# Kernel tuning notes

Hardware: AMD Instinct MI355X
Metric: run time of the kernel (lower is better)

## Reference

```python
import jax, jax.numpy as jnp
import numpy as np

POOL = 7  # pool_size
NUM_ROIS = 512


def setup_inputs() -> dict:
    key = jax.random.key(0)
    k1, k2, k3 = jax.random.split(key, 3)
    img = jax.random.normal(k1, (1, 64, 64, 1024), dtype=jnp.float32)
    xy = jax.random.randint(k2, (NUM_ROIS, 2), 0, 32)   # x1, y1
    wh = jax.random.randint(k3, (NUM_ROIS, 2), 4, 33)   # w, h >= 4 so crops are non-empty
    rois = jnp.concatenate([xy, wh], axis=1).astype(jnp.int32)  # [R,4] (x,y,w,h)
    return {"img": img, "rois": rois}


def _axis_coords(start, eff, pool):
    """Bilinear sample coords for tf.image.resize (half-pixel centers).
    start, eff: [R] int crop origin / effective extent along one axis.
    Returns lo/hi gather indices [R,pool] into the FULL image, and frac [R,pool].
    """
    eff_f = eff.astype(jnp.float32)[:, None]                     # [R,1]
    t = (jnp.arange(pool, dtype=jnp.float32) + 0.5)[None, :] * eff_f / pool - 0.5  # [R,pool]
    f0 = jnp.floor(t)
    frac = t - f0                                                # lerp weight (from unclamped floor, as in TF)
    i0 = jnp.clip(f0, 0.0, eff_f - 1.0).astype(jnp.int32) + start[:, None]
    i1 = jnp.clip(f0 + 1.0, 0.0, eff_f - 1.0).astype(jnp.int32) + start[:, None]
    return i0, i1, frac


def reference(img, rois):
    # img: [B,H,W,C] float32, rois: [R,4] int32 (x,y,w,h). Output: [B,R,P,P,C].
    B, H, W, C = img.shape
    x1, y1, w, h = rois[:, 0], rois[:, 1], rois[:, 2], rois[:, 3]
    we = jnp.minimum(x1 + w, W) - x1   # x2 = min(x1+w, W) as in source
    he = jnp.minimum(y1 + h, H) - y1
    yi0, yi1, fy = _axis_coords(y1, he, POOL)   # [R,P]
    xi0, xi1, fx = _axis_coords(x1, we, POOL)
    # One-shot gather of the 4 bilinear corners for all ROIs/pixels: [B,R,P,P,C]
    v00 = img[:, yi0[:, :, None], xi0[:, None, :], :]
    v01 = img[:, yi0[:, :, None], xi1[:, None, :], :]
    v10 = img[:, yi1[:, :, None], xi0[:, None, :], :]
    v11 = img[:, yi1[:, :, None], xi1[:, None, :], :]
    fx_b = fx[None, :, None, :, None]  # broadcast over [B,R,P(y),P(x),C]
    fy_b = fy[None, :, :, None, None]
    top = v00 + (v01 - v00) * fx_b
    bot = v10 + (v11 - v10) * fx_b
    return top + (bot - top) * fy_b
```

## Files before the change

### kernel.cpp

```cpp
#include <hip/hip_runtime.h>


#define POOLSZ 7
#define NROIS  512
#define IMG_H  64
#define IMG_W  64
#define IMG_C  1024
#define NSLAB  8
#define SLABC  (IMG_C / NSLAB)
#define CELLS  (POOLSZ * POOLSZ)

typedef float fvec4 __attribute__((ext_vector_type(4)));

__global__ __launch_bounds__(256) void roi_pool_slab_kernel(
    const float* __restrict__ img,
    const int*   __restrict__ rois,
    float*       __restrict__ out)
{
    const int bid  = blockIdx.x;
    const int slab = bid & (NSLAB - 1);
    const int r    = bid >> 3;

    const int x1 = rois[r * 4 + 0];
    const int y1 = rois[r * 4 + 1];
    const int w  = rois[r * 4 + 2];
    const int h  = rois[r * 4 + 3];

    const int we = min(x1 + w, IMG_W) - x1;
    const int he = min(y1 + h, IMG_H) - y1;
    const float wef = (float)we;
    const float hef = (float)he;

    const int g    = threadIdx.x >> 5;
    const int lane = threadIdx.x & 31;
    const int c    = slab * SLABC + lane * 4;

    #pragma unroll
    for (int iter = 0; iter < 7; ++iter) {
        const int cell = iter * 8 + g;
        if (cell < CELLS) {
            const int py = cell / POOLSZ;
            const int px = cell % POOLSZ;

            const float ty  = (py + 0.5f) * hef / (float)POOLSZ - 0.5f;
            const float fy0 = floorf(ty);
            const float fy  = ty - fy0;
            const int yi0 = (int)fminf(fmaxf(fy0,        0.0f), hef - 1.0f) + y1;
            const int yi1 = (int)fminf(fmaxf(fy0 + 1.0f, 0.0f), hef - 1.0f) + y1;

            const float tx  = (px + 0.5f) * wef / (float)POOLSZ - 0.5f;
            const float fx0 = floorf(tx);
            const float fx  = tx - fx0;
            const int xi0 = (int)fminf(fmaxf(fx0,        0.0f), wef - 1.0f) + x1;
            const int xi1 = (int)fminf(fmaxf(fx0 + 1.0f, 0.0f), wef - 1.0f) + x1;

            const size_t base00 = ((size_t)(yi0 * IMG_W + xi0)) * IMG_C + c;
            const size_t base01 = ((size_t)(yi0 * IMG_W + xi1)) * IMG_C + c;
            const size_t base10 = ((size_t)(yi1 * IMG_W + xi0)) * IMG_C + c;
            const size_t base11 = ((size_t)(yi1 * IMG_W + xi1)) * IMG_C + c;

            const fvec4 v00 = *reinterpret_cast<const fvec4*>(img + base00);
            const fvec4 v01 = *reinterpret_cast<const fvec4*>(img + base01);
            const fvec4 v10 = *reinterpret_cast<const fvec4*>(img + base10);
            const fvec4 v11 = *reinterpret_cast<const fvec4*>(img + base11);

            const fvec4 top = v00 + (v01 - v00) * fx;
            const fvec4 bot = v10 + (v11 - v10) * fx;
            const fvec4 o   = top + (bot - top) * fy;

            const size_t obase = ((size_t)(r * CELLS + cell)) * IMG_C + c;
            __builtin_nontemporal_store(o, reinterpret_cast<fvec4*>(out + obase));
        }
    }
}

extern "C" void kernel_launch(void* const* d_in, const int* in_sizes, int n_in,
                              void* d_out, int out_size, void* d_ws, size_t ws_size,
                              hipStream_t stream) {
    const float* img  = (const float*)d_in[0];
    const int*   rois = (const int*)d_in[1];
    float*       out  = (float*)d_out;

    const int nblocks = NROIS * NSLAB;
    roi_pool_slab_kernel<<<nblocks, 256, 0, stream>>>(img, rois, out);
}
```

Baseline: 27.63 us.

## Process four ROIs per block with shared-memory precomputed bilinear coordinates

Each block now handles four ROIs for one channel slab, with all 256 threads packed densely over ROI×cell×lane units. The old mapping left the last iteration with only one of eight warp groups active. Per-axis sample indices and lerp fractions are computed once into shared memory instead of per cell per thread. This adds a __syncthreads, shared-memory lookups and integer divides per unit, and cuts the block count by four, which may reduce latency hiding.

Result: faster. 27.05 us (-2.1%).

```diff
diff --git a/kernel.cpp b/kernel.cpp
--- a/kernel.cpp
+++ b/kernel.cpp
@@ -9,50 +9,76 @@
 #define NSLAB  8
 #define SLABC  (IMG_C / NSLAB)
 #define CELLS  (POOLSZ * POOLSZ)
+#define RPB    4
+#define UNITS  (RPB * CELLS * 32)
+#define ITERS  ((UNITS + 255) / 256)
 
 typedef float fvec4 __attribute__((ext_vector_type(4)));
 
-__global__ __launch_bounds__(256) void roi_pool_slab_kernel(
+__global__ __launch_bounds__(256) void roi_pool_kernel(
     const float* __restrict__ img,
     const int*   __restrict__ rois,
     float*       __restrict__ out)
 {
-    const int bid  = blockIdx.x;
-    const int slab = bid & (NSLAB - 1);
-    const int r    = bid >> 3;
+    __shared__ int   sYi0[RPB][POOLSZ], sYi1[RPB][POOLSZ];
+    __shared__ float sFy [RPB][POOLSZ];
+    __shared__ int   sXi0[RPB][POOLSZ], sXi1[RPB][POOLSZ];
+    __shared__ float sFx [RPB][POOLSZ];
 
-    const int x1 = rois[r * 4 + 0];
-    const int y1 = rois[r * 4 + 1];
-    const int w  = rois[r * 4 + 2];
-    const int h  = rois[r * 4 + 3];
+    const int bid     = blockIdx.x;
+    const int slab    = bid & (NSLAB - 1);
+    const int roibase = (bid >> 3) * RPB;
 
-    const int we = min(x1 + w, IMG_W) - x1;
-    const int he = min(y1 + h, IMG_H) - y1;
-    const float wef = (float)we;
-    const float hef = (float)he;
+    const int t = threadIdx.x;
 
-    const int g    = threadIdx.x >> 5;
-    const int lane = threadIdx.x & 31;
-    const int c    = slab * SLABC + lane * 4;
+    if (t < RPB * 2 * POOLSZ) {
+        const int rl   = t / (2 * POOLSZ);
+        const int j    = t % (2 * POOLSZ);
+        const int axis = j / POOLSZ;
+        const int p    = j % POOLSZ;
+        const int r    = roibase + rl;
 
-    #pragma unroll
-    for (int iter = 0; iter < 7; ++iter) {
-        const int cell = iter * 8 + g;
-        if (cell < CELLS) {
-            const int py = cell / POOLSZ;
-            const int px = cell % POOLSZ;
+        const int x1 = rois[r * 4 + 0];
+        const int y1 = rois[r * 4 + 1];
+        const int w  = rois[r * 4 + 2];
+        const int h  = rois[r * 4 + 3];
 
-            const float ty  = (py + 0.5f) * hef / (float)POOLSZ - 0.5f;
-            const float fy0 = floorf(ty);
-            const float fy  = ty - fy0;
-            const int yi0 = (int)fminf(fmaxf(fy0,        0.0f), hef - 1.0f) + y1;
-            const int yi1 = (int)fminf(fmaxf(fy0 + 1.0f, 0.0f), hef - 1.0f) + y1;
+        const int start = axis ? x1 : y1;
+        const int lim   = axis ? IMG_W : IMG_H;
+        const int ext   = axis ? w : h;
+        const int eff   = min(start + ext, lim) - start;
+        const float efff = (float)eff;
 
-            const float tx  = (px + 0.5f) * wef / (float)POOLSZ - 0.5f;
-            const float fx0 = floorf(tx);
-            const float fx  = tx - fx0;
-            const int xi0 = (int)fminf(fmaxf(fx0,        0.0f), wef - 1.0f) + x1;
-            const int xi1 = (int)fminf(fmaxf(fx0 + 1.0f, 0.0f), wef - 1.0f) + x1;
+        const float tq = (p + 0.5f) * efff / (float)POOLSZ - 0.5f;
+        const float f0 = floorf(tq);
+        const float fr = tq - f0;
+        const int i0 = (int)fminf(fmaxf(f0,        0.0f), efff - 1.0f) + start;
+        const int i1 = (int)fminf(fmaxf(f0 + 1.0f, 0.0f), efff - 1.0f) + start;
+
+        if (axis == 0) { sYi0[rl][p] = i0; sYi1[rl][p] = i1; sFy[rl][p] = fr; }
+        else           { sXi0[rl][p] = i0; sXi1[rl][p] = i1; sFx[rl][p] = fr; }
+    }
+    __syncthreads();
+
+    #pragma unroll 5
+    for (int it = 0; it < ITERS; ++it) {
+        const int unit = it * 256 + t;
+        if (unit < UNITS) {
+            const int cellg = unit >> 5;
+            const int lane  = unit & 31;
+            const int rl    = cellg / CELLS;
+            const int cell  = cellg - rl * CELLS;
+            const int py    = cell / POOLSZ;
+            const int px    = cell - py * POOLSZ;
+
+            const int   yi0 = sYi0[rl][py];
+            const int   yi1 = sYi1[rl][py];
+            const float fy  = sFy [rl][py];
+            const int   xi0 = sXi0[rl][px];
+            const int   xi1 = sXi1[rl][px];
+            const float fx  = sFx [rl][px];
+
+            const int c = slab * SLABC + lane * 4;
 
             const size_t base00 = ((size_t)(yi0 * IMG_W + xi0)) * IMG_C + c;
             const size_t base01 = ((size_t)(yi0 * IMG_W + xi1)) * IMG_C + c;
@@ -68,6 +94,7 @@
             const fvec4 bot = v10 + (v11 - v10) * fx;
             const fvec4 o   = top + (bot - top) * fy;
 
+            const int r = roibase + rl;
             const size_t obase = ((size_t)(r * CELLS + cell)) * IMG_C + c;
             __builtin_nontemporal_store(o, reinterpret_cast<fvec4*>(out + obase));
         }
@@ -81,6 +108,6 @@
     const int*   rois = (const int*)d_in[1];
     float*       out  = (float*)d_out;
 
-    const int nblocks = NROIS * NSLAB;
-    roi_pool_slab_kernel<<<nblocks, 256, 0, stream>>>(img, rois, out);
+    const int nblocks = (NROIS / RPB) * NSLAB;
+    roi_pool_kernel<<<nblocks, 256, 0, stream>>>(img, rois, out);
 }
```
